# Kernel tuning notes

Hardware: AMD Instinct MI355X
Metric: run time of the kernel (lower is better)

Reference implementation:

```python
import jax, jax.numpy as jnp
import numpy as np
import math

D_MODEL = 1024
N_HEADS = 16
HEAD_DIM = D_MODEL // N_HEADS
MAX_FUTURE = 128
NEG = -1e20


def setup_inputs() -> dict:
    key = jax.random.key(0)
    ks = jax.random.split(key, 8)
    B, S = 2, 2048
    scale = 1.0 / math.sqrt(D_MODEL)
    return {
        "hidden_states": jax.random.normal(ks[0], (B, S, D_MODEL), dtype=jnp.float32),
        "attention_mask": jnp.ones((B, S), dtype=jnp.int32),
        "Wq": jax.random.normal(ks[1], (D_MODEL, D_MODEL), dtype=jnp.float32) * scale,
        "bq": jnp.zeros((D_MODEL,), dtype=jnp.float32),
        "Wk": jax.random.normal(ks[2], (D_MODEL, D_MODEL), dtype=jnp.float32) * scale,
        "bk": jnp.zeros((D_MODEL,), dtype=jnp.float32),
        "Wv": jax.random.normal(ks[3], (D_MODEL, D_MODEL), dtype=jnp.float32) * scale,
        "bv": jnp.zeros((D_MODEL,), dtype=jnp.float32),
    }


def _split_heads(x):
    # [B, S, D] -> [B, H, S, Dh]
    B, S, _ = x.shape
    return x.reshape(B, S, N_HEADS, HEAD_DIM).transpose(0, 2, 1, 3)


def reference(hidden_states, attention_mask, Wq, bq, Wk, bk, Wv, bv):
    B, S, _ = hidden_states.shape
    q = _split_heads(hidden_states @ Wq.T + bq)
    k = _split_heads(hidden_states @ Wk.T + bk)
    v = _split_heads(hidden_states @ Wv.T + bv)

    # raw scores [B, H, S, S]
    scores = jnp.einsum("bhqd,bhkd->bhqk", q, k)

    # banded ct mask: query i may attend key j iff j <= i + MAX_FUTURE
    i = jnp.arange(S)[:, None]
    j = jnp.arange(S)[None, :]
    ct_mask = (j - MAX_FUTURE) <= i  # [S, S] bool, True = keep
    pad_keep = attention_mask[:, None, None, :] != 0  # [B,1,1,S]

    scores = jnp.where(ct_mask[None, None, :, :], scores, NEG)
    scores = jnp.where(pad_keep, scores, NEG)
    # NOTE: original divides by sqrt(head_dim) AFTER the mask fills
    scores = scores / math.sqrt(HEAD_DIM)

    probs = jax.nn.softmax(scores, axis=-1)
    # dropout prob = 0.0 (eval) -> identity

    ctx = jnp.einsum("bhqk,bhkd->bhqd", probs, v)
    ctx = ctx.transpose(0, 2, 1, 3).reshape(B, S, D_MODEL)
    return ctx, probs
```

## Files before the change

### kernel.cpp

```cpp
#include <hip/hip_runtime.h>
#include <hip/hip_fp16.h>
#include <stdint.h>

typedef _Float16 f16;
typedef f16 f16x8 __attribute__((ext_vector_type(8)));
typedef f16 f16x4 __attribute__((ext_vector_type(4)));
typedef float f32x4 __attribute__((ext_vector_type(4)));

#define S_LEN 2048
#define D_MODEL 1024
#define NH 16
#define HD 64

#define GLOAD_LDS16(g, l)                                                     \
  __builtin_amdgcn_global_load_lds(                                           \
      (const __attribute__((address_space(1))) void*)(g),                     \
      (__attribute__((address_space(3))) void*)(l), 16, 0, 0)

__global__ void k_cvt(const float* __restrict__ src, f16* __restrict__ dst, int n4) {
  int i = blockIdx.x * blockDim.x + threadIdx.x;
  int stride = gridDim.x * blockDim.x;
  for (; i < n4; i += stride) {
    float4 v = ((const float4*)src)[i];
    f16x4 h;
    h[0] = (f16)v.x; h[1] = (f16)v.y; h[2] = (f16)v.z; h[3] = (f16)v.w;
    ((f16x4*)dst)[i] = h;
  }
}

__global__ __launch_bounds__(256) void k_qkv_gemm(
    const f16* __restrict__ X,
    const f16* __restrict__ Wq, const f16* __restrict__ Wk, const f16* __restrict__ Wv,
    const float* __restrict__ bq, const float* __restrict__ bk, const float* __restrict__ bv,
    f16* __restrict__ Qo, f16* __restrict__ Ko, f16* __restrict__ Vt)
{
  const int z = blockIdx.z;
  const f16* W = (z == 0) ? Wq : (z == 1) ? Wk : Wv;
  const float* bias = (z == 0) ? bq : (z == 1) ? bk : bv;

  __shared__ f16 As[128 * 32];
  __shared__ f16 Bs[128 * 32];

  const int tid = threadIdx.x;
  const int lane = tid & 63;
  const int w = tid >> 6;
  const int wm = w >> 1, wn = w & 1;
  const int m0 = blockIdx.y * 128, n0 = blockIdx.x * 128;
  const int lc = lane & 15, kg = lane >> 4;

  f32x4 acc[4][4];
#pragma unroll
  for (int m = 0; m < 4; ++m)
#pragma unroll
    for (int n = 0; n < 4; ++n) acc[m][n] = (f32x4){0.f, 0.f, 0.f, 0.f};

  for (int k0 = 0; k0 < 1024; k0 += 32) {
#pragma unroll
    for (int c = 0; c < 2; ++c) {
      int off = (c * 256 + tid) * 16;
      int row = off >> 6;
      int slot = ((off >> 4) & 3) ^ (row & 3);
      const f16* ga = X + (size_t)(m0 + row) * 1024 + k0 + slot * 8;
      const f16* gb = W + (size_t)(n0 + row) * 1024 + k0 + slot * 8;
      char* la = (char*)As + (c * 256 + w * 64) * 16;
      char* lb = (char*)Bs + (c * 256 + w * 64) * 16;
      GLOAD_LDS16(ga, la);
      GLOAD_LDS16(gb, lb);
    }
    __syncthreads();

    f16x8 af[4], bf[4];
#pragma unroll
    for (int m = 0; m < 4; ++m) {
      int row = wm * 64 + m * 16 + lc;
      int ch = kg ^ (row & 3);
      af[m] = *(const f16x8*)((const char*)As + row * 64 + ch * 16);
    }
#pragma unroll
    for (int n = 0; n < 4; ++n) {
      int row = wn * 64 + n * 16 + lc;
      int ch = kg ^ (row & 3);
      bf[n] = *(const f16x8*)((const char*)Bs + row * 64 + ch * 16);
    }
#pragma unroll
    for (int m = 0; m < 4; ++m)
#pragma unroll
      for (int n = 0; n < 4; ++n)
        acc[m][n] = __builtin_amdgcn_mfma_f32_16x16x32_f16(af[m], bf[n], acc[m][n], 0, 0, 0);
    __syncthreads();
  }

  if (z < 2) {
    f16* O = (z == 0) ? Qo : Ko;
#pragma unroll
    for (int mf = 0; mf < 4; ++mf) {
#pragma unroll
      for (int nf = 0; nf < 4; ++nf) {
        int col = n0 + wn * 64 + nf * 16 + lc;
        float bv_ = bias[col];
        int rbase = m0 + wm * 64 + mf * 16 + kg * 4;
#pragma unroll
        for (int r = 0; r < 4; ++r)
          O[(size_t)(rbase + r) * 1024 + col] = (f16)(acc[mf][nf][r] + bv_);
      }
    }
  } else {
#pragma unroll
    for (int mf = 0; mf < 4; ++mf) {
#pragma unroll
      for (int nf = 0; nf < 4; ++nf) {
        int col = n0 + wn * 64 + nf * 16 + lc;
        float bv_ = bias[col];
        int s_base = m0 + wm * 64 + mf * 16 + kg * 4;
        int b = s_base >> 11;
        int s_loc = s_base & 2047;
        f16x4 pk;
#pragma unroll
        for (int r = 0; r < 4; ++r) pk[r] = (f16)(acc[mf][nf][r] + bv_);
        *(f16x4*)(Vt + (size_t)(b * 1024 + col) * S_LEN + s_loc) = pk;
      }
    }
  }
}

__global__ __launch_bounds__(256) void k_attn(
    const f16* __restrict__ Q, const f16* __restrict__ K, const f16* __restrict__ Vt,
    const int* __restrict__ amask, float* __restrict__ ctx, float* __restrict__ probs)
{
  const int tq = (int)gridDim.x - 1 - (int)blockIdx.x;
  const int h = blockIdx.y, b = blockIdx.z;
  const int bh = b * NH + h;
  const int tid = threadIdx.x, lane = tid & 63, w = tid >> 6;
  const int q0 = tq * 64;
  const int kg = lane >> 4;
  const int lc = lane & 15;

  __shared__ f16 Ks[64 * 64];
  __shared__ f16 Vs[64 * 64];
  __shared__ f16 Ps[4][16 * 64];

  f16x8 qf[2];
  {
    const f16* qb = Q + (size_t)(b * S_LEN + q0 + w * 16 + lc) * D_MODEL + h * HD + kg * 8;
    qf[0] = *(const f16x8*)qb;
    qf[1] = *(const f16x8*)(qb + 32);
  }

  const int n_tiles = (tq + 3 < 32) ? (tq + 3) : 32;
  const int edge_t = tq + 2;

  float m_run[4], l_run[4];
#pragma unroll
  for (int r = 0; r < 4; ++r) { m_run[r] = -3.0e38f; l_run[r] = 0.f; }

  for (int jt = 0; jt < n_tiles; ++jt) {
    const int j0 = jt * 64;
#pragma unroll
    for (int c = 0; c < 2; ++c) {
      int off = (c * 256 + tid) * 16;
      int row = off >> 7;
      int chunk = ((off >> 4) & 7) ^ (row & 7);
      const f16* g = K + (size_t)(b * S_LEN + j0 + row) * D_MODEL + h * HD + chunk * 8;
      GLOAD_LDS16(g, (char*)Ks + (c * 256 + w * 64) * 16);
    }
    __syncthreads();

    bool am[4];
#pragma unroll
    for (int n = 0; n < 4; ++n) am[n] = amask[b * S_LEN + j0 + n * 16 + lc] != 0;

    f32x4 s[4];
#pragma unroll
    for (int n = 0; n < 4; ++n) s[n] = (f32x4){0.f, 0.f, 0.f, 0.f};
#pragma unroll
    for (int ks = 0; ks < 2; ++ks)
#pragma unroll
      for (int n = 0; n < 4; ++n) {
        int row = n * 16 + lc;
        int ch = (ks * 4 + kg) ^ (row & 7);
        f16x8 kf = *(const f16x8*)((const char*)Ks + row * 128 + ch * 16);
        s[n] = __builtin_amdgcn_mfma_f32_16x16x32_f16(qf[ks], kf, s[n], 0, 0, 0);
      }

    const bool edge = (jt == edge_t);
    float sv[4][4], tmax[4];
#pragma unroll
    for (int r = 0; r < 4; ++r) tmax[r] = -3.0e38f;
#pragma unroll
    for (int n = 0; n < 4; ++n) {
      int j = j0 + n * 16 + lc;
#pragma unroll
      for (int r = 0; r < 4; ++r) {
        int i = q0 + w * 16 + kg * 4 + r;
        bool ok = am[n] && (!edge || (j - 128 <= i));
        float v = ok ? s[n][r] * 0.125f : -3.0e38f;
        sv[n][r] = v;
        tmax[r] = fmaxf(tmax[r], v);
      }
    }
#pragma unroll
    for (int m = 1; m < 16; m <<= 1)
#pragma unroll
      for (int r = 0; r < 4; ++r) tmax[r] = fmaxf(tmax[r], __shfl_xor(tmax[r], m));
#pragma unroll
    for (int r = 0; r < 4; ++r) {
      float mn = fmaxf(m_run[r], tmax[r]);
      float corr = __expf(m_run[r] - mn);
      float sum = 0.f;
#pragma unroll
      for (int n = 0; n < 4; ++n) sum += __expf(sv[n][r] - mn);
#pragma unroll
      for (int m = 1; m < 16; m <<= 1) sum += __shfl_xor(sum, m);
      l_run[r] = l_run[r] * corr + sum;
      m_run[r] = mn;
    }
    __syncthreads();
  }

  float inv_l[4];
#pragma unroll
  for (int r = 0; r < 4; ++r) inv_l[r] = 1.f / l_run[r];

  f32x4 opv[4];
#pragma unroll
  for (int n = 0; n < 4; ++n) opv[n] = (f32x4){0.f, 0.f, 0.f, 0.f};

  for (int jt = 0; jt < n_tiles; ++jt) {
    const int j0 = jt * 64;
#pragma unroll
    for (int c = 0; c < 2; ++c) {
      int off = (c * 256 + tid) * 16;
      int row = off >> 7;
      int chunk = ((off >> 4) & 7) ^ (row & 7);
      const f16* gk = K + (size_t)(b * S_LEN + j0 + row) * D_MODEL + h * HD + chunk * 8;
      const f16* gv = Vt + (size_t)(bh * 64 + row) * S_LEN + j0 + chunk * 8;
      GLOAD_LDS16(gk, (char*)Ks + (c * 256 + w * 64) * 16);
      GLOAD_LDS16(gv, (char*)Vs + (c * 256 + w * 64) * 16);
    }
    __syncthreads();

    bool am[4];
#pragma unroll
    for (int n = 0; n < 4; ++n) am[n] = amask[b * S_LEN + j0 + n * 16 + lc] != 0;

    f32x4 s[4];
#pragma unroll
    for (int n = 0; n < 4; ++n) s[n] = (f32x4){0.f, 0.f, 0.f, 0.f};
#pragma unroll
    for (int ks = 0; ks < 2; ++ks)
#pragma unroll
      for (int n = 0; n < 4; ++n) {
        int row = n * 16 + lc;
        int ch = (ks * 4 + kg) ^ (row & 7);
        f16x8 kf = *(const f16x8*)((const char*)Ks + row * 128 + ch * 16);
        s[n] = __builtin_amdgcn_mfma_f32_16x16x32_f16(qf[ks], kf, s[n], 0, 0, 0);
      }

    const bool edge = (jt == edge_t);
#pragma unroll
    for (int n = 0; n < 4; ++n) {
      int j = j0 + n * 16 + lc;
      int colc = n * 2 + (lc >> 3);
#pragma unroll
      for (int r = 0; r < 4; ++r) {
        int i = q0 + w * 16 + kg * 4 + r;
        bool ok = am[n] && (!edge || (j - 128 <= i));
        float p = ok ? __expf(s[n][r] * 0.125f - m_run[r]) * inv_l[r] : 0.f;
        int qrow = kg * 4 + r;
        int cc = colc ^ (qrow & 7);
        *(f16*)((char*)Ps[w] + qrow * 128 + cc * 16 + (lc & 7) * 2) = (f16)p;
      }
    }
    __syncthreads();

#pragma unroll
    for (int ks = 0; ks < 2; ++ks) {
      int ch = (ks * 4 + kg) ^ (lc & 7);
      f16x8 pa = *(const f16x8*)((const char*)Ps[w] + lc * 128 + ch * 16);
#pragma unroll
      for (int n = 0; n < 4; ++n) {
        int vrow = n * 16 + lc;
        int vch = (ks * 4 + kg) ^ (vrow & 7);
        f16x8 vf = *(const f16x8*)((const char*)Vs + vrow * 128 + vch * 16);
        opv[n] = __builtin_amdgcn_mfma_f32_16x16x32_f16(pa, vf, opv[n], 0, 0, 0);
      }
    }

#pragma unroll
    for (int ps = 0; ps < 2; ++ps) {
      int row = ps * 8 + (lane >> 3);
      int ch = (lane & 7) ^ (row & 7);
      f16x8 pv = *(const f16x8*)((const char*)Ps[w] + row * 128 + ch * 16);
      float* dst = probs + (size_t)(bh * S_LEN + q0 + w * 16 + row) * S_LEN + j0 + (lane & 7) * 8;
      *(float4*)dst = make_float4((float)pv[0], (float)pv[1], (float)pv[2], (float)pv[3]);
      *(float4*)(dst + 4) = make_float4((float)pv[4], (float)pv[5], (float)pv[6], (float)pv[7]);
    }
    __syncthreads();
  }

#pragma unroll
  for (int n = 0; n < 4; ++n)
#pragma unroll
    for (int r = 0; r < 4; ++r) {
      int i = q0 + w * 16 + kg * 4 + r;
      ctx[(size_t)(b * S_LEN + i) * D_MODEL + h * HD + n * 16 + lc] = opv[n][r];
    }

  const int jz0 = n_tiles * 64;
  if (jz0 < S_LEN) {
#pragma unroll
    for (int ps = 0; ps < 2; ++ps) {
      int i = q0 + w * 16 + ps * 8 + (lane >> 3);
      float* rowp = probs + (size_t)(bh * S_LEN + i) * S_LEN;
      for (int j = jz0 + (lane & 7) * 4; j < S_LEN; j += 32)
        *(float4*)(rowp + j) = make_float4(0.f, 0.f, 0.f, 0.f);
    }
  }
}

extern "C" void kernel_launch(void* const* d_in, const int* in_sizes, int n_in,
                              void* d_out, int out_size, void* d_ws, size_t ws_size,
                              hipStream_t stream) {
  const float* hidden = (const float*)d_in[0];
  const int* amask = (const int*)d_in[1];
  const float* Wq = (const float*)d_in[2];
  const float* bq = (const float*)d_in[3];
  const float* Wk = (const float*)d_in[4];
  const float* bk = (const float*)d_in[5];
  const float* Wv = (const float*)d_in[6];
  const float* bv = (const float*)d_in[7];

  char* ws = (char*)d_ws;
  f16* Xh  = (f16*)ws; ws += (size_t)4096 * 1024 * 2;
  f16* Wqh = (f16*)ws; ws += (size_t)1024 * 1024 * 2;
  f16* Wkh = (f16*)ws; ws += (size_t)1024 * 1024 * 2;
  f16* Wvh = (f16*)ws; ws += (size_t)1024 * 1024 * 2;
  f16* Qh  = (f16*)ws; ws += (size_t)4096 * 1024 * 2;
  f16* Kh  = (f16*)ws; ws += (size_t)4096 * 1024 * 2;
  f16* Vth = (f16*)ws; ws += (size_t)4096 * 1024 * 2;

  k_cvt<<<1024, 256, 0, stream>>>(hidden, Xh, 4096 * 1024 / 4);
  k_cvt<<<512, 256, 0, stream>>>(Wq, Wqh, 1024 * 1024 / 4);
  k_cvt<<<512, 256, 0, stream>>>(Wk, Wkh, 1024 * 1024 / 4);
  k_cvt<<<512, 256, 0, stream>>>(Wv, Wvh, 1024 * 1024 / 4);

  k_qkv_gemm<<<dim3(8, 32, 3), 256, 0, stream>>>(Xh, Wqh, Wkh, Wvh, bq, bk, bv, Qh, Kh, Vth);

  float* ctx = (float*)d_out;
  float* probs = ctx + (size_t)2 * S_LEN * D_MODEL;
  k_attn<<<dim3(32, 16, 2), 256, 0, stream>>>(Qh, Kh, Vth, amask, ctx, probs);
}
```

Before: 726.8 us.

## Double-buffer K/V tiles, drop online max, fold softmax scale into Q

Folds the 1/sqrt(d)·log2(e) factor into the Q projection so the attention kernel uses exp2 directly. Removes the running-max rescaling in the first pass, computing only a plain exp sum. K and V tiles are double-buffered in LDS so the next tile loads during compute. Probabilities are written straight from registers with nontemporal stores instead of being re-read from LDS. Dropping the max subtraction risks overflow for large scores, and the scalar per-element stores may coalesce less well than the earlier vector stores.

Result: no change. 722.2 us (-0.6%).

```diff
diff --git a/kernel.cpp b/kernel.cpp
--- a/kernel.cpp
+++ b/kernel.cpp
@@ -11,6 +11,7 @@
 #define D_MODEL 1024
 #define NH 16
 #define HD 64
+#define QSCALE 0.18033688011112042f
 
 #define GLOAD_LDS16(g, l)                                                     \
   __builtin_amdgcn_global_load_lds(                                           \
@@ -92,6 +93,7 @@
 
   if (z < 2) {
     f16* O = (z == 0) ? Qo : Ko;
+    const float sc = (z == 0) ? QSCALE : 1.f;
 #pragma unroll
     for (int mf = 0; mf < 4; ++mf) {
 #pragma unroll
@@ -101,7 +103,7 @@
         int rbase = m0 + wm * 64 + mf * 16 + kg * 4;
 #pragma unroll
         for (int r = 0; r < 4; ++r)
-          O[(size_t)(rbase + r) * 1024 + col] = (f16)(acc[mf][nf][r] + bv_);
+          O[(size_t)(rbase + r) * 1024 + col] = (f16)((acc[mf][nf][r] + bv_) * sc);
       }
     }
   } else {
@@ -132,11 +134,10 @@
   const int bh = b * NH + h;
   const int tid = threadIdx.x, lane = tid & 63, w = tid >> 6;
   const int q0 = tq * 64;
-  const int kg = lane >> 4;
-  const int lc = lane & 15;
-
-  __shared__ f16 Ks[64 * 64];
-  __shared__ f16 Vs[64 * 64];
+  const int kg = lane >> 4, lc = lane & 15;
+
+  __shared__ f16 Ks[2][64 * 64];
+  __shared__ f16 Vs[2][64 * 64];
   __shared__ f16 Ps[4][16 * 64];
 
   f16x8 qf[2];
@@ -148,26 +149,41 @@
 
   const int n_tiles = (tq + 3 < 32) ? (tq + 3) : 32;
   const int edge_t = tq + 2;
-
-  float m_run[4], l_run[4];
-#pragma unroll
-  for (int r = 0; r < 4; ++r) { m_run[r] = -3.0e38f; l_run[r] = 0.f; }
-
+  const int* amrow = amask + b * S_LEN;
+
+  int srow[2], schunk[2];
+#pragma unroll
+  for (int c = 0; c < 2; ++c) {
+    int off = (c * 256 + tid) * 16;
+    srow[c] = off >> 7;
+    schunk[c] = ((off >> 4) & 7) ^ (srow[c] & 7);
+  }
+
+#define STAGE_K(JT, BB) do {                                                      \
+    int j0_ = (JT) * 64;                                                          \
+    _Pragma("unroll") for (int c = 0; c < 2; ++c) {                               \
+      const f16* g = K + (size_t)(b * S_LEN + j0_ + srow[c]) * D_MODEL + h * HD + schunk[c] * 8; \
+      GLOAD_LDS16(g, (char*)Ks[BB] + (c * 256 + w * 64) * 16);                    \
+    } } while (0)
+
+#define STAGE_V(JT, BB) do {                                                      \
+    int j0_ = (JT) * 64;                                                          \
+    _Pragma("unroll") for (int c = 0; c < 2; ++c) {                               \
+      const f16* g = Vt + (size_t)(bh * 64 + srow[c]) * S_LEN + j0_ + schunk[c] * 8; \
+      GLOAD_LDS16(g, (char*)Vs[BB] + (c * 256 + w * 64) * 16);                    \
+    } } while (0)
+
+  float lr[4] = {0.f, 0.f, 0.f, 0.f};
+  STAGE_K(0, 0);
   for (int jt = 0; jt < n_tiles; ++jt) {
+    const int cur = jt & 1;
+    __syncthreads();
+    if (jt + 1 < n_tiles) STAGE_K(jt + 1, cur ^ 1);
     const int j0 = jt * 64;
-#pragma unroll
-    for (int c = 0; c < 2; ++c) {
-      int off = (c * 256 + tid) * 16;
-      int row = off >> 7;
-      int chunk = ((off >> 4) & 7) ^ (row & 7);
-      const f16* g = K + (size_t)(b * S_LEN + j0 + row) * D_MODEL + h * HD + chunk * 8;
-      GLOAD_LDS16(g, (char*)Ks + (c * 256 + w * 64) * 16);
-    }
-    __syncthreads();
 
     bool am[4];
 #pragma unroll
-    for (int n = 0; n < 4; ++n) am[n] = amask[b * S_LEN + j0 + n * 16 + lc] != 0;
+    for (int n = 0; n < 4; ++n) am[n] = amrow[j0 + n * 16 + lc] != 0;
 
     f32x4 s[4];
 #pragma unroll
@@ -178,14 +194,11 @@
       for (int n = 0; n < 4; ++n) {
         int row = n * 16 + lc;
         int ch = (ks * 4 + kg) ^ (row & 7);
-        f16x8 kf = *(const f16x8*)((const char*)Ks + row * 128 + ch * 16);
+        f16x8 kf = *(const f16x8*)((const char*)Ks[cur] + row * 128 + ch * 16);
         s[n] = __builtin_amdgcn_mfma_f32_16x16x32_f16(qf[ks], kf, s[n], 0, 0, 0);
       }
 
     const bool edge = (jt == edge_t);
-    float sv[4][4], tmax[4];
-#pragma unroll
-    for (int r = 0; r < 4; ++r) tmax[r] = -3.0e38f;
 #pragma unroll
     for (int n = 0; n < 4; ++n) {
       int j = j0 + n * 16 + lc;
@@ -193,55 +206,39 @@
       for (int r = 0; r < 4; ++r) {
         int i = q0 + w * 16 + kg * 4 + r;
         bool ok = am[n] && (!edge || (j - 128 <= i));
-        float v = ok ? s[n][r] * 0.125f : -3.0e38f;
-        sv[n][r] = v;
-        tmax[r] = fmaxf(tmax[r], v);
-      }
-    }
-#pragma unroll
-    for (int m = 1; m < 16; m <<= 1)
-#pragma unroll
-      for (int r = 0; r < 4; ++r) tmax[r] = fmaxf(tmax[r], __shfl_xor(tmax[r], m));
-#pragma unroll
-    for (int r = 0; r < 4; ++r) {
-      float mn = fmaxf(m_run[r], tmax[r]);
-      float corr = __expf(m_run[r] - mn);
-      float sum = 0.f;
-#pragma unroll
-      for (int n = 0; n < 4; ++n) sum += __expf(sv[n][r] - mn);
-#pragma unroll
-      for (int m = 1; m < 16; m <<= 1) sum += __shfl_xor(sum, m);
-      l_run[r] = l_run[r] * corr + sum;
-      m_run[r] = mn;
-    }
+        float e = __builtin_amdgcn_exp2f(s[n][r]);
+        lr[r] += ok ? e : 0.f;
+      }
+    }
+  }
+#pragma unroll
+  for (int m = 1; m < 16; m <<= 1)
+#pragma unroll
+    for (int r = 0; r < 4; ++r) lr[r] += __shfl_xor(lr[r], m);
+  float inv_l[4];
+  float* prow[4];
+#pragma unroll
+  for (int r = 0; r < 4; ++r) {
+    inv_l[r] = 1.f / lr[r];
+    prow[r] = probs + ((size_t)bh * S_LEN + q0 + w * 16 + kg * 4 + r) * S_LEN;
+  }
+
+  f32x4 opv[4];
+#pragma unroll
+  for (int n = 0; n < 4; ++n) opv[n] = (f32x4){0.f, 0.f, 0.f, 0.f};
+
+  __syncthreads();
+  STAGE_K(0, 0);
+  STAGE_V(0, 0);
+  for (int jt = 0; jt < n_tiles; ++jt) {
+    const int cur = jt & 1;
     __syncthreads();
-  }
-
-  float inv_l[4];
-#pragma unroll
-  for (int r = 0; r < 4; ++r) inv_l[r] = 1.f / l_run[r];
-
-  f32x4 opv[4];
-#pragma unroll
-  for (int n = 0; n < 4; ++n) opv[n] = (f32x4){0.f, 0.f, 0.f, 0.f};
-
-  for (int jt = 0; jt < n_tiles; ++jt) {
+    if (jt + 1 < n_tiles) { STAGE_K(jt + 1, cur ^ 1); STAGE_V(jt + 1, cur ^ 1); }
     const int j0 = jt * 64;
-#pragma unroll
-    for (int c = 0; c < 2; ++c) {
-      int off = (c * 256 + tid) * 16;
-      int row = off >> 7;
-      int chunk = ((off >> 4) & 7) ^ (row & 7);
-      const f16* gk = K + (size_t)(b * S_LEN + j0 + row) * D_MODEL + h * HD + chunk * 8;
-      const f16* gv = Vt + (size_t)(bh * 64 + row) * S_LEN + j0 + chunk * 8;
-      GLOAD_LDS16(gk, (char*)Ks + (c * 256 + w * 64) * 16);
-      GLOAD_LDS16(gv, (char*)Vs + (c * 256 + w * 64) * 16);
-    }
-    __syncthreads();
 
     bool am[4];
 #pragma unroll
-    for (int n = 0; n < 4; ++n) am[n] = amask[b * S_LEN + j0 + n * 16 + lc] != 0;
+    for (int n = 0; n < 4; ++n) am[n] = amrow[j0 + n * 16 + lc] != 0;
 
     f32x4 s[4];
 #pragma unroll
@@ -252,7 +249,7 @@
       for (int n = 0; n < 4; ++n) {
         int row = n * 16 + lc;
         int ch = (ks * 4 + kg) ^ (row & 7);
-        f16x8 kf = *(const f16x8*)((const char*)Ks + row * 128 + ch * 16);
+        f16x8 kf = *(const f16x8*)((const char*)Ks[cur] + row * 128 + ch * 16);
         s[n] = __builtin_amdgcn_mfma_f32_16x16x32_f16(qf[ks], kf, s[n], 0, 0, 0);
       }
 
@@ -265,13 +262,15 @@
       for (int r = 0; r < 4; ++r) {
         int i = q0 + w * 16 + kg * 4 + r;
         bool ok = am[n] && (!edge || (j - 128 <= i));
-        float p = ok ? __expf(s[n][r] * 0.125f - m_run[r]) * inv_l[r] : 0.f;
+        float p = ok ? __builtin_amdgcn_exp2f(s[n][r]) * inv_l[r] : 0.f;
+        __builtin_nontemporal_store(p, prow[r] + j);
         int qrow = kg * 4 + r;
         int cc = colc ^ (qrow & 7);
         *(f16*)((char*)Ps[w] + qrow * 128 + cc * 16 + (lc & 7) * 2) = (f16)p;
       }
     }
-    __syncthreads();
+    asm volatile("s_waitcnt lgkmcnt(0)" ::: "memory");
+    __builtin_amdgcn_sched_barrier(0);
 
 #pragma unroll
     for (int ks = 0; ks < 2; ++ks) {
@@ -281,21 +280,10 @@
       for (int n = 0; n < 4; ++n) {
         int vrow = n * 16 + lc;
         int vch = (ks * 4 + kg) ^ (vrow & 7);
-        f16x8 vf = *(const f16x8*)((const char*)Vs + vrow * 128 + vch * 16);
+        f16x8 vf = *(const f16x8*)((const char*)Vs[cur] + vrow * 128 + vch * 16);
         opv[n] = __builtin_amdgcn_mfma_f32_16x16x32_f16(pa, vf, opv[n], 0, 0, 0);
       }
     }
-
-#pragma unroll
-    for (int ps = 0; ps < 2; ++ps) {
-      int row = ps * 8 + (lane >> 3);
-      int ch = (lane & 7) ^ (row & 7);
-      f16x8 pv = *(const f16x8*)((const char*)Ps[w] + row * 128 + ch * 16);
-      float* dst = probs + (size_t)(bh * S_LEN + q0 + w * 16 + row) * S_LEN + j0 + (lane & 7) * 8;
-      *(float4*)dst = make_float4((float)pv[0], (float)pv[1], (float)pv[2], (float)pv[3]);
-      *(float4*)(dst + 4) = make_float4((float)pv[4], (float)pv[5], (float)pv[6], (float)pv[7]);
-    }
-    __syncthreads();
   }
 
 #pragma unroll
@@ -303,19 +291,23 @@
 #pragma unroll
     for (int r = 0; r < 4; ++r) {
       int i = q0 + w * 16 + kg * 4 + r;
-      ctx[(size_t)(b * S_LEN + i) * D_MODEL + h * HD + n * 16 + lc] = opv[n][r];
+      __builtin_nontemporal_store(
+          opv[n][r], ctx + (size_t)(b * S_LEN + i) * D_MODEL + h * HD + n * 16 + lc);
     }
 
   const int jz0 = n_tiles * 64;
   if (jz0 < S_LEN) {
+    f32x4 z4 = (f32x4){0.f, 0.f, 0.f, 0.f};
 #pragma unroll
     for (int ps = 0; ps < 2; ++ps) {
       int i = q0 + w * 16 + ps * 8 + (lane >> 3);
-      float* rowp = probs + (size_t)(bh * S_LEN + i) * S_LEN;
+      float* rowp = probs + ((size_t)bh * S_LEN + i) * S_LEN;
       for (int j = jz0 + (lane & 7) * 4; j < S_LEN; j += 32)
-        *(float4*)(rowp + j) = make_float4(0.f, 0.f, 0.f, 0.f);
-    }
-  }
+        __builtin_nontemporal_store(z4, (f32x4*)(rowp + j));
+    }
+  }
+#undef STAGE_K
+#undef STAGE_V
 }
 
 extern "C" void kernel_launch(void* const* d_in, const int* in_sizes, int n_in,
```
